# Kernel tuning notes

Hardware: AMD Instinct MI355X
Metric: run time of the kernel (lower is better)

## Reference

```python
import jax, jax.numpy as jnp
import numpy as np

B, S, D, H = 2, 2048, 1024, 16
HD = D // H
NEG = -1000000000.0


def setup_inputs() -> dict:
    key = jax.random.key(0)
    k1, k2, k3, k4, k5, k6, k7 = jax.random.split(key, 7)
    scale = 1.0 / np.sqrt(D)
    return {
        "q": jax.random.normal(k1, (B, S, D), jnp.float32),
        "k": jax.random.normal(k2, (B, S, D), jnp.float32),
        "v": jax.random.normal(k3, (B, S, D), jnp.float32),
        # causal mask, broadcastable over (B, H, S, S)
        "mask": jnp.tril(jnp.ones((S, S), jnp.bool_))[None, None, :, :],
        "Wq": jax.random.normal(k4, (D, D), jnp.float32) * scale,
        "Wk": jax.random.normal(k5, (D, D), jnp.float32) * scale,
        "Wv": jax.random.normal(k6, (D, D), jnp.float32) * scale,
        "Wo": jax.random.normal(k7, (D, D), jnp.float32) * scale,
    }


def reference(q, k, v, mask, Wq, Wk, Wv, Wo):
    # nn.Linear(bias=False): y = x @ W.T
    qp = jnp.einsum("bsd,ed->bse", q, Wq).reshape(B, S, H, HD).transpose(0, 2, 1, 3)
    kp = jnp.einsum("bsd,ed->bse", k, Wk).reshape(B, S, H, HD).transpose(0, 2, 1, 3)
    vp = jnp.einsum("bsd,ed->bse", v, Wv).reshape(B, S, H, HD).transpose(0, 2, 1, 3)
    # scaled dot-product attention with masked softmax (dropout p=0)
    scores = jnp.einsum("bhqd,bhkd->bhqk", qp, kp) / jnp.sqrt(jnp.float32(HD))
    scores = jnp.where(mask, scores, NEG)
    attn = jax.nn.softmax(scores, axis=-1)
    ctx = jnp.einsum("bhqk,bhkd->bhqd", attn, vp)
    ctx = ctx.transpose(0, 2, 1, 3).reshape(B, S, D)
    return jnp.einsum("bsd,ed->bse", ctx, Wo)
```

## Files before the change

### kernel.cpp

```cpp
#include <hip/hip_runtime.h>

typedef __bf16 bf16;
typedef __bf16 bf16x4 __attribute__((ext_vector_type(4)));
typedef __bf16 bf16x8 __attribute__((ext_vector_type(8)));
typedef float f32x4 __attribute__((ext_vector_type(4)));
typedef float f32x16 __attribute__((ext_vector_type(16)));
typedef unsigned u32x4 __attribute__((ext_vector_type(4)));

static constexpr int Bn = 2, Sn = 2048, Dn = 1024, Hn = 16, HDn = 64;

__device__ __forceinline__ void gload_lds16(const void* g, void* l) {
  __builtin_amdgcn_global_load_lds((__attribute__((address_space(1))) void*)g,
                                   (__attribute__((address_space(3))) void*)l, 16, 0, 0);
}

__device__ __forceinline__ f32x4 mfma_bf16_16x16x32(bf16x8 a, bf16x8 b, f32x4 c) {
  return __builtin_amdgcn_mfma_f32_16x16x32_bf16(a, b, c, 0, 0, 0);
}

__device__ __forceinline__ f32x16 mfma_bf16_32x32x16(bf16x8 a, bf16x8 b, f32x16 c) {
  return __builtin_amdgcn_mfma_f32_32x32x16_bf16(a, b, c, 0, 0, 0);
}

__device__ __forceinline__ float fast_exp2(float x) {
  float r;
  asm("v_exp_f32 %0, %1" : "=v"(r) : "v"(x));
  return r;
}

__device__ __forceinline__ unsigned cvt_pk_bf16(float lo, float hi) {
  unsigned r;
  asm("v_cvt_pk_bf16_f32 %0, %1, %2" : "=v"(r) : "v"(lo), "v"(hi));
  return r;
}

__device__ __forceinline__ float cross_half_max(float v) {
  return fmaxf(v, __shfl_xor(v, 32, 64));
}
__device__ __forceinline__ float cross_half_add(float v) {
  return v + __shfl_xor(v, 32, 64);
}
__device__ __forceinline__ unsigned shfl32u(unsigned u) {
  return (unsigned)__shfl_xor((int)u, 32, 64);
}

#define WAITCNT_VM(N) asm volatile("s_waitcnt vmcnt(" #N ")" ::: "memory")
#define WAITCNT_LGKM0 asm volatile("s_waitcnt lgkmcnt(0)" ::: "memory")

struct CvtArgs {
  const float* in[7];
  bf16* out[7];
  int n4[7];
  float sc[7];
};

__global__ __launch_bounds__(256) void cvt_all(CvtArgs a) {
  const float* in = a.in[blockIdx.z];
  bf16* out = a.out[blockIdx.z];
  const int n4 = a.n4[blockIdx.z];
  const float s = a.sc[blockIdx.z];
  int i = blockIdx.x * 256 + threadIdx.x;
  const int stride = gridDim.x * 256;
  for (; i < n4; i += stride) {
    float4 v = reinterpret_cast<const float4*>(in)[i];
    bf16x4 o;
    o[0] = (bf16)(v.x * s); o[1] = (bf16)(v.y * s);
    o[2] = (bf16)(v.z * s); o[3] = (bf16)(v.w * s);
    reinterpret_cast<bf16x4*>(out)[i] = o;
  }
}

__device__ __forceinline__ void store_out(float* C, size_t i, float v) { C[i] = v; }
__device__ __forceinline__ void store_out(bf16* C, size_t i, float v) { C[i] = (bf16)v; }

template <typename OutT>
__device__ __forceinline__ void gemm_bt_dev(const bf16* __restrict__ A,
                                            const bf16* __restrict__ Bw,
                                            OutT* __restrict__ C,
                                            int K, int N, int row0, int col0) {
  const int t = threadIdx.x;
  const int l = t & 63, w = t >> 6;
  const int wr = w >> 1, wc = w & 1;
  const int lc = l & 15, lg = l >> 4;

  __shared__ bf16 As[128 * 32];
  __shared__ bf16 Bs[128 * 32];

  f32x4 acc[4][4] = {};

  for (int k0 = 0; k0 < K; k0 += 32) {
#pragma unroll
    for (int i = 0; i < 2; ++i) {
      const int c = i * 256 + t;
      const int r = c >> 2;
      const int scc = (c & 3) ^ (r & 3);
      gload_lds16(A + (size_t)(row0 + r) * K + k0 + scc * 8, As + c * 8);
      gload_lds16(Bw + (size_t)(col0 + r) * K + k0 + scc * 8, Bs + c * 8);
    }
    __syncthreads();

    bf16x8 af[4], bfr[4];
#pragma unroll
    for (int m = 0; m < 4; ++m) {
      const int r = wr * 64 + m * 16 + lc;
      af[m] = *reinterpret_cast<const bf16x8*>(As + r * 32 + ((lg ^ (r & 3)) * 8));
    }
#pragma unroll
    for (int n = 0; n < 4; ++n) {
      const int r = wc * 64 + n * 16 + lc;
      bfr[n] = *reinterpret_cast<const bf16x8*>(Bs + r * 32 + ((lg ^ (r & 3)) * 8));
    }
#pragma unroll
    for (int m = 0; m < 4; ++m)
#pragma unroll
      for (int n = 0; n < 4; ++n)
        acc[m][n] = mfma_bf16_16x16x32(af[m], bfr[n], acc[m][n]);
    __syncthreads();
  }

#pragma unroll
  for (int m = 0; m < 4; ++m) {
    const int rbase = row0 + wr * 64 + m * 16 + lg * 4;
#pragma unroll
    for (int n = 0; n < 4; ++n) {
      const int col = col0 + wc * 64 + n * 16 + lc;
#pragma unroll
      for (int j = 0; j < 4; ++j)
        store_out(C, (size_t)(rbase + j) * N + col, acc[m][n][j]);
    }
  }
}

__global__ __launch_bounds__(256) void gemm_qkv(
    const bf16* __restrict__ qa, const bf16* __restrict__ wq, bf16* __restrict__ qo,
    const bf16* __restrict__ ka, const bf16* __restrict__ wk, bf16* __restrict__ ko,
    const bf16* __restrict__ va, const bf16* __restrict__ wv, bf16* __restrict__ vo) {
  const int n = blockIdx.x;
  const int orig = (n & 7) * 96 + (n >> 3);
  const int x = orig & 7, y = (orig >> 3) & 31, z = orig >> 8;
  const bf16 *A, *Bw;
  bf16* C;
  if (z == 0)      { A = qa; Bw = wq; C = qo; }
  else if (z == 1) { A = ka; Bw = wk; C = ko; }
  else             { A = va; Bw = wv; C = vo; }
  gemm_bt_dev<bf16>(A, Bw, C, Dn, Dn, y * 128, x * 128);
}

__global__ __launch_bounds__(256) void gemm_out_f32(const bf16* __restrict__ A,
                                                    const bf16* __restrict__ Bw,
                                                    float* __restrict__ C) {
  const int n = blockIdx.x;
  const int orig = (n & 7) * 32 + (n >> 3);
  const int x = orig & 7, y = orig >> 3;
  gemm_bt_dev<float>(A, Bw, C, Dn, Dn, y * 128, x * 128);
}

__global__ __launch_bounds__(256) void transpose_bsd(const bf16* __restrict__ in,
                                                     bf16* __restrict__ out) {
  __shared__ bf16 tile[64][66];
  const int s0 = blockIdx.x * 64, d0 = blockIdx.y * 64, b = blockIdx.z;
  const int t = threadIdx.x;
#pragma unroll
  for (int i = 0; i < 2; ++i) {
    const int c = i * 256 + t;
    const int r = c >> 3, cc = (c & 7) * 8;
    const bf16x8 v = *reinterpret_cast<const bf16x8*>(
        in + ((size_t)b * Sn + s0 + r) * Dn + d0 + cc);
#pragma unroll
    for (int j = 0; j < 8; ++j) tile[r][cc + j] = v[j];
  }
  __syncthreads();
#pragma unroll
  for (int i = 0; i < 2; ++i) {
    const int c = i * 256 + t;
    const int r = c >> 3, cc = (c & 7) * 8;
    bf16x8 v;
#pragma unroll
    for (int j = 0; j < 8; ++j) v[j] = tile[cc + j][r];
    *reinterpret_cast<bf16x8*>(out + ((size_t)b * Dn + d0 + r) * Sn + s0 + cc) = v;
  }
}

__global__ __launch_bounds__(512) void flash_attn(const bf16* __restrict__ qp,
                                                  const bf16* __restrict__ kp,
                                                  const bf16* __restrict__ vt,
                                                  bf16* __restrict__ ctx) {
  const int n = blockIdx.x;
  const int g = (n & 7) + 8 * (n >> 6);
  const int pid = (n >> 3) & 7;
  const int h = g & 15;
  const int b = g >> 4;
  const int t = threadIdx.x, w = t >> 6, l = t & 63;
  const int lq = l & 31, hi = l >> 5;
  const int half = w >> 2;

  __shared__ char smem[81920];
  char* my = smem + half * 40960;

  const int tl = t & 255;
  const int rl = tl >> 3;
  const int scc = (tl & 7) ^ (rl & 7);
  const bf16* kbase = kp + ((size_t)b * Sn + rl) * Dn + h * HDn + scc * 8;
  const bf16* vbase = vt + ((size_t)b * Dn + h * HDn + rl) * Sn + scc * 8;

  for (int ph = 0; ph < 2; ++ph) {
    const int qt = ph ? pid : 15 - pid;
    const int qrow0 = qt * 128 + (w & 3) * 32;
    const int cnt = qt + 1;
    const int tbase = half * cnt;

    auto STAGE = [&](int i) {
      const int kv0 = (tbase + i) * 64;
      char* Kd = my + (i & 1) * 8192 + tl * 16;
      char* Vd = my + 16384 + (i % 3) * 8192 + tl * 16;
      const bf16* ks = kbase + (size_t)kv0 * Dn;
      const bf16* vs = vbase + kv0;
#pragma unroll
      for (int ii = 0; ii < 2; ++ii) {
        gload_lds16(ks + (size_t)ii * 32 * Dn, Kd + ii * 4096);
        gload_lds16(vs + (size_t)ii * 32 * Sn, Vd + ii * 4096);
      }
    };

    bf16x8 qf[4];
#pragma unroll
    for (int kk = 0; kk < 4; ++kk)
      qf[kk] = *reinterpret_cast<const bf16x8*>(
          qp + ((size_t)b * Sn + qrow0 + lq) * Dn + h * HDn + kk * 16 + hi * 8);

    f32x16 oacc0 = {}, oacc1 = {};
    float mrow = -1e30f, lsum = 0.0f;

    auto QK = [&](int i, f32x16& s0_, f32x16& s1_) {
      const char* Kc = my + (i & 1) * 8192;
      __builtin_amdgcn_s_setprio(1);
#pragma unroll
      for (int kk = 0; kk < 4; ++kk) {
        const int ch = kk * 2 + hi;
        const int r0 = lq, r1 = 32 + lq;
        const bf16x8 k0 = *reinterpret_cast<const bf16x8*>(Kc + r0 * 128 + ((ch ^ (r0 & 7)) << 4));
        const bf16x8 k1 = *reinterpret_cast<const bf16x8*>(Kc + r1 * 128 + ((ch ^ (r1 & 7)) << 4));
        s0_ = mfma_bf16_32x32x16(k0, qf[kk], s0_);
        s1_ = mfma_bf16_32x32x16(k1, qf[kk], s1_);
      }
      __builtin_amdgcn_s_setprio(0);
    };

    auto SMPV = [&](int i, f32x16& s0, f32x16& s1) {
      const int kv0 = (tbase + i) * 64;
      const char* Vc = my + 16384 + (i % 3) * 8192;

      if (kv0 + 63 > qrow0) {
        const int qg = qrow0 + lq;
#pragma unroll
        for (int r = 0; r < 16; ++r) {
          const int kvl = (r & 3) + 8 * (r >> 2) + 4 * hi;
          if (kv0 + kvl > qg)      s0[r] = -1e30f;
          if (kv0 + 32 + kvl > qg) s1[r] = -1e30f;
        }
      }

      float mx[8];
#pragma unroll
      for (int i2 = 0; i2 < 8; ++i2)
        mx[i2] = fmaxf(fmaxf(s0[i2], s0[i2 + 8]), fmaxf(s1[i2], s1[i2 + 8]));
#pragma unroll
      for (int i2 = 0; i2 < 4; ++i2) mx[i2] = fmaxf(mx[i2], mx[i2 + 4]);
      const float tmax_own = fmaxf(fmaxf(mx[0], mx[1]), fmaxf(mx[2], mx[3]));
      const float tmax = cross_half_max(tmax_own);

      float alpha = 1.0f;
      if (!__all(tmax <= mrow + 8.0f)) {
        const float mn = fmaxf(mrow, tmax);
        alpha = fast_exp2(mrow - mn);
        mrow = mn;
#pragma unroll
        for (int r = 0; r < 16; ++r) { oacc0[r] *= alpha; oacc1[r] *= alpha; }
      }
#pragma unroll
      for (int r = 0; r < 16; ++r) {
        s0[r] = fast_exp2(s0[r] - mrow);
        s1[r] = fast_exp2(s1[r] - mrow);
      }
      float sm[8];
#pragma unroll
      for (int i2 = 0; i2 < 8; ++i2)
        sm[i2] = (s0[i2] + s0[i2 + 8]) + (s1[i2] + s1[i2 + 8]);
#pragma unroll
      for (int i2 = 0; i2 < 4; ++i2) sm[i2] += sm[i2 + 4];
      float rsum = (sm[0] + sm[1]) + (sm[2] + sm[3]);
      rsum = cross_half_add(rsum);
      lsum = lsum * alpha + rsum;

      u32x4 pw[4];
#pragma unroll
      for (int c2 = 0; c2 < 4; ++c2) {
        const f32x16& S = (c2 < 2) ? s0 : s1;
        const int base = (c2 & 1) * 8;
        const unsigned u0 = cvt_pk_bf16(S[base + 0], S[base + 1]);
        const unsigned u1 = cvt_pk_bf16(S[base + 2], S[base + 3]);
        const unsigned u2 = cvt_pk_bf16(S[base + 4], S[base + 5]);
        const unsigned u3 = cvt_pk_bf16(S[base + 6], S[base + 7]);
        const unsigned r1 = shfl32u(hi ? u0 : u2);
        const unsigned r2 = shfl32u(hi ? u1 : u3);
        pw[c2][0] = hi ? r1 : u0;
        pw[c2][1] = hi ? r2 : u1;
        pw[c2][2] = hi ? u2 : r1;
        pw[c2][3] = hi ? u3 : r2;
      }

      __builtin_amdgcn_s_setprio(1);
#pragma unroll
      for (int kk = 0; kk < 4; ++kk) {
        const bf16x8 pf = __builtin_bit_cast(bf16x8, pw[kk]);
        const int ch = kk * 2 + hi;
        const int r0 = lq, r1 = 32 + lq;
        const bf16x8 v0 = *reinterpret_cast<const bf16x8*>(Vc + r0 * 128 + ((ch ^ (r0 & 7)) << 4));
        const bf16x8 v1 = *reinterpret_cast<const bf16x8*>(Vc + r1 * 128 + ((ch ^ (r1 & 7)) << 4));
        oacc0 = mfma_bf16_32x32x16(v0, pf, oacc0);
        oacc1 = mfma_bf16_32x32x16(v1, pf, oacc1);
      }
      __builtin_amdgcn_s_setprio(0);
    };

    __builtin_amdgcn_s_barrier();
    __builtin_amdgcn_sched_barrier(0);

    STAGE(0);
    if (cnt > 1) { STAGE(1); WAITCNT_VM(4); } else { WAITCNT_VM(0); }
    __builtin_amdgcn_sched_barrier(0);
    __builtin_amdgcn_s_barrier();
    __builtin_amdgcn_sched_barrier(0);

    f32x16 sp0 = {}, sp1 = {};
    if (tbase * 64 <= qrow0 + 31) QK(0, sp0, sp1);

    for (int i = 0; i < cnt; ++i) {
      WAITCNT_VM(0);
      __builtin_amdgcn_sched_barrier(0);
      __builtin_amdgcn_s_barrier();
      __builtin_amdgcn_sched_barrier(0);

      if (i + 2 < cnt) STAGE(i + 2);
      f32x16 sn0 = {}, sn1 = {};
      if (i + 1 < cnt && (tbase + i + 1) * 64 <= qrow0 + 31) QK(i + 1, sn0, sn1);
      if ((tbase + i) * 64 <= qrow0 + 31) SMPV(i, sp0, sp1);
      sp0 = sn0; sp1 = sn1;
      WAITCNT_LGKM0;
    }

    __builtin_amdgcn_s_barrier();
    __builtin_amdgcn_sched_barrier(0);

    float* Op = (float*)smem;
    float* Ml = (float*)(smem + 33280);
    const int lrow = (w & 3) * 32 + lq;

    if (half == 1) {
#pragma unroll
      for (int r = 0; r < 16; ++r) {
        const int d = (r & 3) + 8 * (r >> 2) + 4 * hi;
        Op[lrow * 65 + d]      = oacc0[r];
        Op[lrow * 65 + 32 + d] = oacc1[r];
      }
      if (hi == 0) { Ml[lrow] = mrow; Ml[128 + lrow] = lsum; }
    }
    WAITCNT_LGKM0;
    __builtin_amdgcn_s_barrier();
    __builtin_amdgcn_sched_barrier(0);

    if (half == 0) {
      const float m1 = Ml[lrow], l1 = Ml[128 + lrow];
      const float mm = fmaxf(mrow, m1);
      const float a0 = fast_exp2(mrow - mm);
      const float a1 = fast_exp2(m1 - mm);
      const float inv = 1.0f / (lsum * a0 + l1 * a1);

      bf16* ep = (bf16*)(smem + 40960 + w * 4608);
#pragma unroll
      for (int dt = 0; dt < 2; ++dt) {
        const f32x16& O = dt ? oacc1 : oacc0;
#pragma unroll
        for (int g2 = 0; g2 < 4; ++g2) {
          bf16x4 o4;
#pragma unroll
          for (int jj = 0; jj < 4; ++jj) {
            const int d = dt * 32 + 8 * g2 + 4 * hi + jj;
            const float o1 = Op[lrow * 65 + d];
            o4[jj] = (bf16)((O[g2 * 4 + jj] * a0 + o1 * a1) * inv);
          }
          const int d0 = dt * 32 + g2 * 8 + hi * 4;
          *reinterpret_cast<bf16x4*>(&ep[lq * 72 + d0]) = o4;
        }
      }
      WAITCNT_LGKM0;
      __builtin_amdgcn_sched_barrier(0);
#pragma unroll
      for (int i = 0; i < 4; ++i) {
        const int q = i * 8 + (l >> 3);
        const int d0 = (l & 7) * 8;
        const bf16x8 vv = *reinterpret_cast<const bf16x8*>(&ep[q * 72 + d0]);
        *reinterpret_cast<bf16x8*>(
            &ctx[((size_t)b * Sn + qrow0 + q) * Dn + h * HDn + d0]) = vv;
      }
    }
  }
}

extern "C" void kernel_launch(void* const* d_in, const int* in_sizes, int n_in,
                              void* d_out, int out_size, void* d_ws, size_t ws_size,
                              hipStream_t stream) {
  const float* q  = (const float*)d_in[0];
  const float* k  = (const float*)d_in[1];
  const float* v  = (const float*)d_in[2];
  const float* Wq = (const float*)d_in[4];
  const float* Wk = (const float*)d_in[5];
  const float* Wv = (const float*)d_in[6];
  const float* Wo = (const float*)d_in[7];

  constexpr size_t BSD = (size_t)Bn * Sn * Dn;
  constexpr size_t DD  = (size_t)Dn * Dn;

  char* p = (char*)d_ws;
  bf16* qbf = (bf16*)p; p += BSD * 2;
  bf16* kbf = (bf16*)p; p += BSD * 2;
  bf16* vbf = (bf16*)p; p += BSD * 2;
  bf16* qpb = (bf16*)p; p += BSD * 2;
  bf16* kpb = (bf16*)p; p += BSD * 2;
  bf16* vpb = (bf16*)p; p += BSD * 2;
  bf16* wqb = (bf16*)p; p += DD * 2;
  bf16* wkb = (bf16*)p; p += DD * 2;
  bf16* wvb = (bf16*)p; p += DD * 2;
  bf16* wob = (bf16*)p; p += DD * 2;
  bf16* vtb  = kbf;
  bf16* ctxb = qbf;

  const float wq_scale = 0.125f * 1.4426950408889634f;

  CvtArgs ca;
  ca.in[0] = q;  ca.out[0] = qbf; ca.n4[0] = (int)(BSD / 4); ca.sc[0] = 1.0f;
  ca.in[1] = k;  ca.out[1] = kbf; ca.n4[1] = (int)(BSD / 4); ca.sc[1] = 1.0f;
  ca.in[2] = v;  ca.out[2] = vbf; ca.n4[2] = (int)(BSD / 4); ca.sc[2] = 1.0f;
  ca.in[3] = Wq; ca.out[3] = wqb; ca.n4[3] = (int)(DD / 4);  ca.sc[3] = wq_scale;
  ca.in[4] = Wk; ca.out[4] = wkb; ca.n4[4] = (int)(DD / 4);  ca.sc[4] = 1.0f;
  ca.in[5] = Wv; ca.out[5] = wvb; ca.n4[5] = (int)(DD / 4);  ca.sc[5] = 1.0f;
  ca.in[6] = Wo; ca.out[6] = wob; ca.n4[6] = (int)(DD / 4);  ca.sc[6] = 1.0f;
  cvt_all<<<dim3(1024, 1, 7), 256, 0, stream>>>(ca);

  gemm_qkv<<<dim3(768), 256, 0, stream>>>(
      qbf, wqb, qpb, kbf, wkb, kpb, vbf, wvb, vpb);

  transpose_bsd<<<dim3(Sn / 64, Dn / 64, Bn), 256, 0, stream>>>(vpb, vtb);

  flash_attn<<<dim3(256), 512, 0, stream>>>(qpb, kpb, vtb, ctxb);

  gemm_out_f32<<<dim3(256), 256, 0, stream>>>(ctxb, wob, (float*)d_out);

  (void)in_sizes; (void)n_in; (void)out_size; (void)ws_size;
}
```

Measured before the change: 120.1 us.

## Split-K output projection across two half-blocks with LDS reduction

```diff
diff --git a/kernel.cpp b/kernel.cpp
--- a/kernel.cpp
+++ b/kernel.cpp
@@ -146,13 +146,89 @@
   gemm_bt_dev<bf16>(A, Bw, C, Dn, Dn, y * 128, x * 128);
 }
 
-__global__ __launch_bounds__(256) void gemm_out_f32(const bf16* __restrict__ A,
+__global__ __launch_bounds__(512) void gemm_out_f32(const bf16* __restrict__ A,
                                                     const bf16* __restrict__ Bw,
                                                     float* __restrict__ C) {
   const int n = blockIdx.x;
   const int orig = (n & 7) * 32 + (n >> 3);
   const int x = orig & 7, y = orig >> 3;
-  gemm_bt_dev<float>(A, Bw, C, Dn, Dn, y * 128, x * 128);
+  const int row0 = y * 128, col0 = x * 128;
+
+  const int t = threadIdx.x;
+  const int half = t >> 8;
+  const int tl = t & 255;
+  const int l = tl & 63, wl = tl >> 6;
+  const int wr = wl >> 1, wc = wl & 1;
+  const int lc = l & 15, lg = l >> 4;
+
+  __shared__ char smem[65536];
+  bf16* As = (bf16*)(smem + half * 16384);
+  bf16* Bs = (bf16*)(smem + half * 16384 + 8192);
+
+  f32x4 acc[4][4] = {};
+  const int kbase = half * 512;
+
+  for (int k0i = 0; k0i < 512; k0i += 32) {
+    const int k0 = kbase + k0i;
+#pragma unroll
+    for (int i = 0; i < 2; ++i) {
+      const int c = i * 256 + tl;
+      const int r = c >> 2;
+      const int scc = (c & 3) ^ (r & 3);
+      gload_lds16(A + (size_t)(row0 + r) * Dn + k0 + scc * 8, As + c * 8);
+      gload_lds16(Bw + (size_t)(col0 + r) * Dn + k0 + scc * 8, Bs + c * 8);
+    }
+    __syncthreads();
+
+    bf16x8 af[4], bfr[4];
+#pragma unroll
+    for (int m = 0; m < 4; ++m) {
+      const int r = wr * 64 + m * 16 + lc;
+      af[m] = *reinterpret_cast<const bf16x8*>(As + r * 32 + ((lg ^ (r & 3)) * 8));
+    }
+#pragma unroll
+    for (int nn = 0; nn < 4; ++nn) {
+      const int r = wc * 64 + nn * 16 + lc;
+      bfr[nn] = *reinterpret_cast<const bf16x8*>(Bs + r * 32 + ((lg ^ (r & 3)) * 8));
+    }
+#pragma unroll
+    for (int m = 0; m < 4; ++m)
+#pragma unroll
+      for (int nn = 0; nn < 4; ++nn)
+        acc[m][nn] = mfma_bf16_16x16x32(af[m], bfr[nn], acc[m][nn]);
+    __syncthreads();
+  }
+
+  float* Op = (float*)smem;
+  if (half == 1) {
+#pragma unroll
+    for (int m = 0; m < 4; ++m) {
+      const int rl = wr * 64 + m * 16 + lg * 4;
+#pragma unroll
+      for (int nn = 0; nn < 4; ++nn) {
+        const int cl = wc * 64 + nn * 16 + lc;
+#pragma unroll
+        for (int j = 0; j < 4; ++j)
+          Op[(rl + j) * 128 + cl] = acc[m][nn][j];
+      }
+    }
+  }
+  __syncthreads();
+
+  if (half == 0) {
+#pragma unroll
+    for (int m = 0; m < 4; ++m) {
+      const int rl = wr * 64 + m * 16 + lg * 4;
+#pragma unroll
+      for (int nn = 0; nn < 4; ++nn) {
+        const int cl = wc * 64 + nn * 16 + lc;
+#pragma unroll
+        for (int j = 0; j < 4; ++j)
+          C[(size_t)(row0 + rl + j) * Dn + col0 + cl] =
+              acc[m][nn][j] + Op[(rl + j) * 128 + cl];
+      }
+    }
+  }
 }
 
 __global__ __launch_bounds__(256) void transpose_bsd(const bf16* __restrict__ in,
@@ -454,7 +530,7 @@
 
   flash_attn<<<dim3(256), 512, 0, stream>>>(qpb, kpb, vtb, ctxb);
 
-  gemm_out_f32<<<dim3(256), 256, 0, stream>>>(ctxb, wob, (float*)d_out);
+  gemm_out_f32<<<dim3(256), 512, 0, stream>>>(ctxb, wob, (float*)d_out);
 
   (void)in_sizes; (void)n_in; (void)out_size; (void)ws_size;
 }
```

Result: faster. 116.8 us (-2.8%).
